# Kernel tuning notes

Hardware: AMD Instinct MI355X
Metric: run time of the kernel (lower is better)

The kernel has to match this reference:

```python
import jax, jax.numpy as jnp
import numpy as np

B, F, R, C, D = 512, 784, 512, 16, 49  # batch, in_features, in_regions, out_channels, dimension
N_REP, N_PART = 32, 16                 # 32 repetitions x 16 partitions = 512 regions
HALF_LOG_2PI = float(0.5 * np.log(2.0 * np.pi))


def setup_inputs() -> dict:
    key = jax.random.key(0)
    k1, k2, k3 = jax.random.split(key, 3)
    # regions: each repetition is a random permutation of the 784 features
    # split into 16 contiguous chunks of 49 -> mask has shape [R, D]
    rng = np.random.default_rng(0)
    mask = np.stack([rng.permutation(F).reshape(N_PART, D) for _ in range(N_REP)])
    mask = mask.reshape(R, D)
    x = jax.random.normal(k1, (B, F), dtype=jnp.float32)
    loc = 0.1 * jax.random.normal(k2, (R, C, D), dtype=jnp.float32)
    scale = 0.5 + 0.05 * jax.random.normal(k3, (R, C, D), dtype=jnp.float32)
    return {"x": x, "mask": jnp.asarray(mask, dtype=jnp.int32), "loc": loc, "scale": scale}


def reference(x, mask, loc, scale):
    # gather features per region: [B, R, D]
    xg = x[:, mask]
    # broadcast against [R, C, D] leaf params -> [B, R, C, D]
    z = (xg[:, :, None, :] - loc) / scale
    logp = -0.5 * z * z - jnp.log(scale) - HALF_LOG_2PI
    # NaN inputs mark marginalized variables -> contribute log-prob 0
    logp = jnp.where(jnp.isnan(logp), jnp.zeros((), logp.dtype), logp)
    # pad == 0 for this config, so no pad_mask branch
    return jnp.sum(logp, axis=-1)  # [B, R, C]
```

## Files before the change

### kernel.cpp

```cpp
#include <hip/hip_runtime.h>
#include <math.h>

#define B_ 512
#define F_ 784
#define R_ 512
#define C_ 16
#define D_ 49
#define HALF_LOG_2PI 0.9189385332046727f

typedef float v2f __attribute__((ext_vector_type(2)));


__global__ __launch_bounds__(256) void k_transpose(const float* __restrict__ x,
                                                   float* __restrict__ xT) {
  int i = blockIdx.x * 256 + threadIdx.x;
  int b = i / F_;
  int f = i - b * F_;
  xT[f * B_ + b] = x[i];
}

__global__ __launch_bounds__(256) void k_coeff(const float* __restrict__ loc,
                                               const float* __restrict__ scale,
                                               float* __restrict__ PQ,
                                               float* __restrict__ Kc) {
  int i = blockIdx.x * 256 + threadIdx.x;
  int r = i >> 4;
  int c = i & 15;
  float kacc = 0.f;
  for (int d = 0; d < D_; ++d) {
    float l = loc[i * D_ + d];
    float s = scale[i * D_ + d];
    float P = 0.f, Q = 0.f;
    bool valid = (s > 0.f) && isfinite(s) && isfinite(l);
    if (valid) {
      float inv  = 1.f / s;
      float inv2 = inv * inv;
      P = -0.5f * inv2;
      Q = l * inv2;
      kacc += -0.5f * l * l * inv2 - logf(s) - HALF_LOG_2PI;
    }
    PQ[(r * D_ + d) * 32 + c]      = P;
    PQ[(r * D_ + d) * 32 + 16 + c] = Q;
  }
  Kc[i] = kacc;
}

__global__ __launch_bounds__(256) void k_main(const float* __restrict__ xT,
                                              const float* __restrict__ PQ,
                                              const float* __restrict__ Kc,
                                              const int* __restrict__ mask,
                                              float* __restrict__ out) {
  const int r = blockIdx.x;
  const int t = threadIdx.x;

  __shared__ float sPQ[D_ * 32];
  __shared__ int   sM[D_];

  for (int i = t; i < D_ * 32; i += 256) sPQ[i] = PQ[r * (D_ * 32) + i];
  if (t < D_) sM[t] = mask[r * D_ + t];

  v2f acc[C_];
#pragma unroll
  for (int c = 0; c < C_; ++c) {
    float k = Kc[r * C_ + c];
    acc[c] = (v2f){k, k};
  }
  __syncthreads();

  const int b0 = 2 * t;

#pragma unroll 7
  for (int d = 0; d < D_; ++d) {
    const v2f xv  = *(const v2f*)&xT[sM[d] * B_ + b0];
    const v2f xv2 = xv * xv;
    const float* pq = &sPQ[d * 32];
#pragma unroll
    for (int c = 0; c < C_; ++c) {
      float P = pq[c], Q = pq[16 + c];
      acc[c] = __builtin_elementwise_fma((v2f){P, P}, xv2, acc[c]);
      acc[c] = __builtin_elementwise_fma((v2f){Q, Q}, xv, acc[c]);
    }
  }

  float4* o0 = (float4*)&out[((size_t)b0 * R_ + r) * C_];
  float4* o1 = (float4*)&out[(((size_t)b0 + 1) * R_ + r) * C_];
#pragma unroll
  for (int q = 0; q < 4; ++q) {
    o0[q] = make_float4(acc[4*q+0].x, acc[4*q+1].x, acc[4*q+2].x, acc[4*q+3].x);
    o1[q] = make_float4(acc[4*q+0].y, acc[4*q+1].y, acc[4*q+2].y, acc[4*q+3].y);
  }
}

extern "C" void kernel_launch(void* const* d_in, const int* in_sizes, int n_in,
                              void* d_out, int out_size, void* d_ws, size_t ws_size,
                              hipStream_t stream) {
  const float* x     = (const float*)d_in[0];
  const int*   mask  = (const int*)  d_in[1];
  const float* loc   = (const float*)d_in[2];
  const float* scale = (const float*)d_in[3];
  float* out = (float*)d_out;

  float* ws = (float*)d_ws;
  float* xT = ws;
  float* PQ = xT + F_ * B_;
  float* Kc = PQ + R_ * D_ * 32;

  hipLaunchKernelGGL(k_transpose, dim3((B_ * F_) / 256), dim3(256), 0, stream, x, xT);
  hipLaunchKernelGGL(k_coeff, dim3((R_ * C_) / 256), dim3(256), 0, stream,
                     loc, scale, PQ, Kc);
  hipLaunchKernelGGL(k_main, dim3(R_), dim3(256), 0, stream, xT, PQ, Kc, mask, out);
}
```

Measured before the change: 110.9 us.

## Tile transpose via LDS, parallelize coeff precompute, read PQ directly in main

The transpose now goes through a padded 32x33 shared tile so that both its reads and its writes are coalesced. The coefficient kernel now runs one block per region with coalesced loads and a shared-memory reduction, replacing the old 32-block launch whose threads each looped over strided data. The main kernel drops its LDS staging and __syncthreads and instead reads PQ as uniform float4 loads and the mask straight from global memory. This relies on those uniform loads being cached or scalarized, at some risk of extra global traffic per iteration.

```diff
diff --git a/kernel.cpp b/kernel.cpp
--- a/kernel.cpp
+++ b/kernel.cpp
@@ -13,36 +13,52 @@
 
 __global__ __launch_bounds__(256) void k_transpose(const float* __restrict__ x,
                                                    float* __restrict__ xT) {
-  int i = blockIdx.x * 256 + threadIdx.x;
-  int b = i / F_;
-  int f = i - b * F_;
-  xT[f * B_ + b] = x[i];
+  __shared__ float tile[32][33];
+  const int tx = threadIdx.x & 31;
+  const int ty = threadIdx.x >> 5;
+  const int f0 = blockIdx.x * 32;
+  const int b0 = blockIdx.y * 32;
+#pragma unroll
+  for (int j = 0; j < 4; ++j) {
+    int b = b0 + ty + j * 8;
+    if (f0 + tx < F_) tile[ty + j * 8][tx] = x[b * F_ + f0 + tx];
+  }
+  __syncthreads();
+#pragma unroll
+  for (int j = 0; j < 4; ++j) {
+    int f = f0 + ty + j * 8;
+    if (f < F_) xT[(size_t)f * B_ + b0 + tx] = tile[tx][ty + j * 8];
+  }
 }
 
 __global__ __launch_bounds__(256) void k_coeff(const float* __restrict__ loc,
                                                const float* __restrict__ scale,
                                                float* __restrict__ PQ,
                                                float* __restrict__ Kc) {
-  int i = blockIdx.x * 256 + threadIdx.x;
-  int r = i >> 4;
-  int c = i & 15;
-  float kacc = 0.f;
-  for (int d = 0; d < D_; ++d) {
-    float l = loc[i * D_ + d];
-    float s = scale[i * D_ + d];
-    float P = 0.f, Q = 0.f;
+  const int r = blockIdx.x;
+  const int t = threadIdx.x;
+  __shared__ float sTerm[C_ * D_];
+  float* pqr = PQ + (size_t)r * (D_ * 32);
+
+  for (int e = t; e < C_ * D_; e += 256) {
+    float l = loc[(size_t)r * C_ * D_ + e];
+    float s = scale[(size_t)r * C_ * D_ + e];
+    int c = e / D_;
+    int d = e - c * D_;
     bool valid = (s > 0.f) && isfinite(s) && isfinite(l);
-    if (valid) {
-      float inv  = 1.f / s;
-      float inv2 = inv * inv;
-      P = -0.5f * inv2;
-      Q = l * inv2;
-      kacc += -0.5f * l * l * inv2 - logf(s) - HALF_LOG_2PI;
-    }
-    PQ[(r * D_ + d) * 32 + c]      = P;
-    PQ[(r * D_ + d) * 32 + 16 + c] = Q;
+    float inv2 = valid ? 1.f / (s * s) : 0.f;
+    float P = -0.5f * inv2;
+    float Q = l * inv2;
+    pqr[d * 32 + c] = P;
+    pqr[d * 32 + 16 + c] = Q;
+    sTerm[e] = valid ? (-0.5f * l * l * inv2 - __logf(s) - HALF_LOG_2PI) : 0.f;
   }
-  Kc[i] = kacc;
+  __syncthreads();
+  if (t < C_) {
+    float k = 0.f;
+    for (int d = 0; d < D_; ++d) k += sTerm[t * D_ + d];
+    Kc[r * C_ + t] = k;
+  }
 }
 
 __global__ __launch_bounds__(256) void k_main(const float* __restrict__ xT,
@@ -52,33 +68,37 @@
                                               float* __restrict__ out) {
   const int r = blockIdx.x;
   const int t = threadIdx.x;
+  const int b0 = 2 * t;
 
-  __shared__ float sPQ[D_ * 32];
-  __shared__ int   sM[D_];
-
-  for (int i = t; i < D_ * 32; i += 256) sPQ[i] = PQ[r * (D_ * 32) + i];
-  if (t < D_) sM[t] = mask[r * D_ + t];
+  const float* __restrict__ pqr = PQ + (size_t)r * (D_ * 32);
+  const int* __restrict__ mr = mask + r * D_;
+  const float* __restrict__ kr = Kc + r * C_;
 
   v2f acc[C_];
 #pragma unroll
   for (int c = 0; c < C_; ++c) {
-    float k = Kc[r * C_ + c];
+    float k = kr[c];
     acc[c] = (v2f){k, k};
   }
-  __syncthreads();
-
-  const int b0 = 2 * t;
 
 #pragma unroll 7
   for (int d = 0; d < D_; ++d) {
-    const v2f xv  = *(const v2f*)&xT[sM[d] * B_ + b0];
+    const int f = mr[d];
+    const v2f xv = *(const v2f*)&xT[(size_t)f * B_ + b0];
     const v2f xv2 = xv * xv;
-    const float* pq = &sPQ[d * 32];
+    const float4* pq4 = (const float4*)(pqr + d * 32);
 #pragma unroll
-    for (int c = 0; c < C_; ++c) {
-      float P = pq[c], Q = pq[16 + c];
-      acc[c] = __builtin_elementwise_fma((v2f){P, P}, xv2, acc[c]);
-      acc[c] = __builtin_elementwise_fma((v2f){Q, Q}, xv, acc[c]);
+    for (int g = 0; g < 4; ++g) {
+      float4 P = pq4[g];
+      float4 Q = pq4[4 + g];
+      acc[4*g+0] = __builtin_elementwise_fma((v2f){P.x, P.x}, xv2,
+                   __builtin_elementwise_fma((v2f){Q.x, Q.x}, xv, acc[4*g+0]));
+      acc[4*g+1] = __builtin_elementwise_fma((v2f){P.y, P.y}, xv2,
+                   __builtin_elementwise_fma((v2f){Q.y, Q.y}, xv, acc[4*g+1]));
+      acc[4*g+2] = __builtin_elementwise_fma((v2f){P.z, P.z}, xv2,
+                   __builtin_elementwise_fma((v2f){Q.z, Q.z}, xv, acc[4*g+2]));
+      acc[4*g+3] = __builtin_elementwise_fma((v2f){P.w, P.w}, xv2,
+                   __builtin_elementwise_fma((v2f){Q.w, Q.w}, xv, acc[4*g+3]));
     }
   }
 
@@ -105,8 +125,7 @@
   float* PQ = xT + F_ * B_;
   float* Kc = PQ + R_ * D_ * 32;
 
-  hipLaunchKernelGGL(k_transpose, dim3((B_ * F_) / 256), dim3(256), 0, stream, x, xT);
-  hipLaunchKernelGGL(k_coeff, dim3((R_ * C_) / 256), dim3(256), 0, stream,
-                     loc, scale, PQ, Kc);
+  hipLaunchKernelGGL(k_transpose, dim3(25, 16), dim3(256), 0, stream, x, xT);
+  hipLaunchKernelGGL(k_coeff, dim3(R_), dim3(256), 0, stream, loc, scale, PQ, Kc);
   hipLaunchKernelGGL(k_main, dim3(R_), dim3(256), 0, stream, xT, PQ, Kc, mask, out);
 }
```

Result: faster. 107.5 us (-3.1%).
